# Optimization experiments

Measured on AMD Instinct MI355X. Metric: run time of the kernel, lower is better.

The kernel has to match this reference:

```python
import jax, jax.numpy as jnp
import numpy as np

NEG_INF = -1e9


def _gru_cell(x, h, W_ih, W_hh, b_ih, b_hh):
    # torch GRUCell math, gate order [r; z; n]
    gx = x @ W_ih.T + b_ih          # [B, 3H]
    gh = h @ W_hh.T + b_hh          # [B, 3H]
    xr, xz, xn = jnp.split(gx, 3, axis=-1)
    hr, hz, hn = jnp.split(gh, 3, axis=-1)
    r = jax.nn.sigmoid(xr + hr)
    z = jax.nn.sigmoid(xz + hz)
    n = jnp.tanh(xn + r * hn)
    return (1.0 - z) * n + z * h


def setup_inputs() -> dict:
    key = jax.random.key(0)
    ks = jax.random.split(key, 8)
    B, N, D, H, P = 64, 2048, 256, 256, 256
    s = 0.05
    return {
        "sequence": jax.random.normal(ks[0], (B, N, D), jnp.float32),
        "hidden_t": jax.random.normal(ks[1], (B, H), jnp.float32),
        "sequence_mask": jnp.ones((B, N), jnp.float32),
        "num_steps": 2,
        "W_seq": jax.random.normal(ks[2], (D, P), jnp.float32) * s,
        "W_h": jax.random.normal(ks[3], (H, P), jnp.float32) * s,
        "v_att": jax.random.normal(ks[4], (P,), jnp.float32) * s,
        "W_ih": jax.random.normal(ks[5], (3 * H, D), jnp.float32) * s,
        "W_hh": jax.random.normal(ks[6], (3 * H, H), jnp.float32) * s,
        "b_ih": jnp.zeros((3 * H,), jnp.float32),
        "b_hh": jnp.zeros((3 * H,), jnp.float32),
    }


def reference(sequence, hidden_t, sequence_mask, num_steps,
              W_seq, W_h, v_att, W_ih, W_hh, b_ih, b_hh):
    # Precompute the sequence projection once (invariant across decode steps).
    seq_proj = jnp.einsum("bnd,dp->bnp", sequence, W_seq)   # [B, N, P]
    mask_bias = jnp.where(sequence_mask > 0, 0.0, NEG_INF)  # [B, N]

    def step(h, _):
        # projection similarity: v . tanh(W1 s_i + W2 h)
        proj = jnp.tanh(seq_proj + (h @ W_h)[:, None, :])   # [B, N, P]
        scores = jnp.einsum("bnp,p->bn", proj, v_att) + mask_bias
        w = jax.nn.softmax(scores, axis=-1)                  # [B, N]
        vec = jnp.einsum("bn,bnd->bd", w, sequence)          # [B, D]
        h_new = _gru_cell(vec, h, W_ih, W_hh, b_ih, b_hh)
        return h_new, w

    _, ws = jax.lax.scan(step, hidden_t, None, length=num_steps)  # [T, B, N]
    return jnp.transpose(ws, (1, 0, 2))                            # [B, T, N]
```

## Files before the change

### kernel.cpp

```cpp
#include <hip/hip_runtime.h>
#include <cstdint>

using u16 = unsigned short;
using u32 = unsigned int;
typedef __attribute__((ext_vector_type(8))) short bf16x8;
typedef __attribute__((ext_vector_type(8))) u16 u16x8;
typedef __attribute__((ext_vector_type(16))) float f32x16;
typedef __attribute__((ext_vector_type(2))) u32 u32x2;
typedef __attribute__((ext_vector_type(4))) u32 u32x4;

#define DEV static __device__ __forceinline__

DEV u16 bf16_rne(float x) {
  u32 u = __float_as_uint(x);
  u32 r = (u + 0x7FFFu + ((u >> 16) & 1u)) >> 16;
  return (u16)r;
}
DEV float bf16f(u16 h) { return __uint_as_float(((u32)h) << 16); }

DEV u32 cvt_pk_bf16(float lo, float hi) {
  u32 d;
  asm("v_cvt_pk_bf16_f32 %0, %1, %2" : "=v"(d) : "v"(lo), "v"(hi));
  return d;
}

DEV float fast_tanh(float x) {
  float e = __expf(2.0f * x);
  return fmaf(-2.0f, __builtin_amdgcn_rcpf(e + 1.0f), 1.0f);
}
DEV float sigmoidf_(float x) {
  return __builtin_amdgcn_rcpf(1.0f + __expf(-x));
}

__global__ __launch_bounds__(256) void prep_all(
    const float* __restrict__ Wseq, const float* __restrict__ Wih,
    const float* __restrict__ Whh, u16* __restrict__ WfG,
    float* __restrict__ WT, float* __restrict__ UT,
    const float* __restrict__ h0, const float* __restrict__ Wh,
    float* __restrict__ hw) {
  const int bid = blockIdx.x, t = threadIdx.x;
  if (bid < 32) {
    const int unit = bid * 4 + (t >> 6);
    const int lane = t & 63, l31 = lane & 31, koct = lane >> 5;
    const int pt8 = unit >> 4, kt = unit & 15;
    u16x8 o;
#pragma unroll
    for (int e = 0; e < 8; ++e)
      o[e] = bf16_rne(
          Wseq[(long)(kt * 16 + koct * 8 + e) * 256 + pt8 * 32 + l31]);
    *(u16x8*)(WfG + (long)unit * 512 + lane * 8) = o;
  } else if (bid < 56) {
    const int gid = bid - 32;
    const float* src = (gid >= 12) ? Whh : Wih;
    float* dst = (gid >= 12) ? UT : WT;
    const int g = (gid % 12) * 64 + (t & 63);
    const int dq = t >> 6;
#pragma unroll 4
    for (int d = dq * 64; d < dq * 64 + 64; ++d)
      dst[(long)d * 768 + g] = src[(long)g * 256 + d];
  } else {
    const int idx = bid - 56;
    const int q = idx & 3, b = idx >> 2;
    __shared__ float sh[256];
    __shared__ float sP[4][64];
    sh[t] = h0[b * 256 + t];
    __syncthreads();
    const int j4 = t & 63, dg = t >> 6;
    const int j = q * 64 + j4;
    float g = 0.f;
#pragma unroll 4
    for (int k = dg * 64; k < dg * 64 + 64; ++k)
      g = fmaf(sh[k], Wh[(long)k * 256 + j], g);
    sP[dg][j4] = g;
    __syncthreads();
    if (t < 64)
      hw[b * 256 + q * 64 + t] = (sP[0][t] + sP[1][t]) + (sP[2][t] + sP[3][t]);
  }
}

__global__ __launch_bounds__(256) void hw_q(const float* __restrict__ h,
                                            const float* __restrict__ Wh,
                                            float* __restrict__ hw) {
  const int q = blockIdx.x, b = blockIdx.y, t = threadIdx.x;
  __shared__ float sh[256];
  __shared__ float sP[4][64];
  sh[t] = h[b * 256 + t];
  __syncthreads();
  const int j4 = t & 63, dg = t >> 6;
  const int j = q * 64 + j4;
  float g = 0.f;
#pragma unroll 4
  for (int k = dg * 64; k < dg * 64 + 64; ++k)
    g = fmaf(sh[k], Wh[(long)k * 256 + j], g);
  sP[dg][j4] = g;
  __syncthreads();
  if (t < 64)
    hw[b * 256 + q * 64 + t] = (sP[0][t] + sP[1][t]) + (sP[2][t] + sP[3][t]);
}

struct EpiSmem {
  float sQ[128][5];
  float se[128];
  float shw[256];
  float svv[256];
  float sredE[2];
};

template <bool FROMLDS>
DEV void epilogue(EpiSmem& sm, const f32x16& a00, const f32x16& a01,
                  const f32x16& a10, const f32x16& a11, const u16* bs,
                  const char* sRb, const float* __restrict__ mask,
                  float* __restrict__ wbuf, float* __restrict__ esum,
                  float* __restrict__ part, long nbase, int esumIdx,
                  long partBase, int t, int lane, int w, int l31, int koct,
                  int pg, int ng) {
  float s0a = 0.f, s0b = 0.f, s0c = 0.f, s0d = 0.f;
  float s1a = 0.f, s1b = 0.f, s1c = 0.f, s1d = 0.f;
#pragma unroll
  for (int r = 0; r < 16; r += 4) {
    const int c0 = (r & 3) + 8 * (r >> 2) + 4 * koct;
    const int c1 = ((r + 1) & 3) + 8 * ((r + 1) >> 2) + 4 * koct;
    const int c2 = ((r + 2) & 3) + 8 * ((r + 2) >> 2) + 4 * koct;
    const int c3 = ((r + 3) & 3) + 8 * ((r + 3) >> 2) + 4 * koct;
    const int p0 = pg * 64 + c0, p1 = pg * 64 + c1, p2 = pg * 64 + c2,
              p3 = pg * 64 + c3;
    s0a = fmaf(sm.svv[p0], fast_tanh(a00[r] + sm.shw[p0]), s0a);
    s0b = fmaf(sm.svv[p1], fast_tanh(a00[r + 1] + sm.shw[p1]), s0b);
    s0c = fmaf(sm.svv[p2], fast_tanh(a00[r + 2] + sm.shw[p2]), s0c);
    s0d = fmaf(sm.svv[p3], fast_tanh(a00[r + 3] + sm.shw[p3]), s0d);
    s1a = fmaf(sm.svv[p0], fast_tanh(a01[r] + sm.shw[p0]), s1a);
    s1b = fmaf(sm.svv[p1], fast_tanh(a01[r + 1] + sm.shw[p1]), s1b);
    s1c = fmaf(sm.svv[p2], fast_tanh(a01[r + 2] + sm.shw[p2]), s1c);
    s1d = fmaf(sm.svv[p3], fast_tanh(a01[r + 3] + sm.shw[p3]), s1d);
  }
#pragma unroll
  for (int r = 0; r < 16; r += 4) {
    const int c0 = (r & 3) + 8 * (r >> 2) + 4 * koct;
    const int c1 = ((r + 1) & 3) + 8 * ((r + 1) >> 2) + 4 * koct;
    const int c2 = ((r + 2) & 3) + 8 * ((r + 2) >> 2) + 4 * koct;
    const int c3 = ((r + 3) & 3) + 8 * ((r + 3) >> 2) + 4 * koct;
    const int p0 = pg * 64 + 32 + c0, p1 = pg * 64 + 32 + c1,
              p2 = pg * 64 + 32 + c2, p3 = pg * 64 + 32 + c3;
    s0a = fmaf(sm.svv[p0], fast_tanh(a10[r] + sm.shw[p0]), s0a);
    s0b = fmaf(sm.svv[p1], fast_tanh(a10[r + 1] + sm.shw[p1]), s0b);
    s0c = fmaf(sm.svv[p2], fast_tanh(a10[r + 2] + sm.shw[p2]), s0c);
    s0d = fmaf(sm.svv[p3], fast_tanh(a10[r + 3] + sm.shw[p3]), s0d);
    s1a = fmaf(sm.svv[p0], fast_tanh(a11[r] + sm.shw[p0]), s1a);
    s1b = fmaf(sm.svv[p1], fast_tanh(a11[r + 1] + sm.shw[p1]), s1b);
    s1c = fmaf(sm.svv[p2], fast_tanh(a11[r + 2] + sm.shw[p2]), s1c);
    s1d = fmaf(sm.svv[p3], fast_tanh(a11[r + 3] + sm.shw[p3]), s1d);
  }
  float sc0 = (s0a + s0b) + (s0c + s0d);
  float sc1 = (s1a + s1b) + (s1c + s1d);
  sc0 += __shfl_xor(sc0, 32, 64);
  sc1 += __shfl_xor(sc1, 32, 64);
  if (koct == 0) {
    sm.sQ[ng * 64 + l31][pg] = sc0;
    sm.sQ[ng * 64 + 32 + l31][pg] = sc1;
  }
  __syncthreads();
  if (t < 128) {
    float s = (sm.sQ[t][0] + sm.sQ[t][1]) + (sm.sQ[t][2] + sm.sQ[t][3]);
    const long n = nbase + t;
    float e = (mask[n] > 0.f) ? __expf(s) : 0.f;
    sm.se[t] = e;
    wbuf[n] = e;
    float s4 = e;
#pragma unroll
    for (int off = 1; off < 64; off <<= 1) s4 += __shfl_xor(s4, off, 64);
    if ((t & 63) == 0) sm.sredE[t >> 6] = s4;
  }
  __syncthreads();
  if (t == 0) esum[esumIdx] = sm.sredE[0] + sm.sredE[1];

#pragma unroll
  for (int kk = 0; kk < 2; ++kk) {
    const int kt = w + kk * 8;
    float vd0 = 0, vd1 = 0, vd2 = 0, vd3 = 0, vd4 = 0, vd5 = 0, vd6 = 0,
          vd7 = 0;
#pragma unroll
    for (int t8 = 0; t8 < 4; ++t8) {
      u16x8 q;
      if constexpr (FROMLDS) {
        const int row = t8 * 32 + l31;
        const int colb = (kt * 16 + koct * 8) * 2;
        q = *(const u16x8*)(sRb + row * 512 + (colb ^ ((row & 31) << 4)));
      } else {
        q = *(const u16x8*)(bs + ((long)(t8 * 16 + kt) * 64 + lane) * 8);
      }
      const float wv = sm.se[t8 * 32 + l31];
      vd0 = fmaf(wv, bf16f((u16)q[0]), vd0);
      vd1 = fmaf(wv, bf16f((u16)q[1]), vd1);
      vd2 = fmaf(wv, bf16f((u16)q[2]), vd2);
      vd3 = fmaf(wv, bf16f((u16)q[3]), vd3);
      vd4 = fmaf(wv, bf16f((u16)q[4]), vd4);
      vd5 = fmaf(wv, bf16f((u16)q[5]), vd5);
      vd6 = fmaf(wv, bf16f((u16)q[6]), vd6);
      vd7 = fmaf(wv, bf16f((u16)q[7]), vd7);
    }
#pragma unroll
    for (int off = 1; off < 32; off <<= 1) {
      vd0 += __shfl_xor(vd0, off, 64);
      vd1 += __shfl_xor(vd1, off, 64);
      vd2 += __shfl_xor(vd2, off, 64);
      vd3 += __shfl_xor(vd3, off, 64);
      vd4 += __shfl_xor(vd4, off, 64);
      vd5 += __shfl_xor(vd5, off, 64);
      vd6 += __shfl_xor(vd6, off, 64);
      vd7 += __shfl_xor(vd7, off, 64);
    }
    if (l31 == 0) {
      float4 o0 = {vd0, vd1, vd2, vd3};
      float4 o1 = {vd4, vd5, vd6, vd7};
      float* pp = part + partBase * 256 + kt * 16 + koct * 8;
      *(float4*)pp = o0;
      *(float4*)(pp + 4) = o1;
    }
  }
}

__global__ __launch_bounds__(512, 4) void step0k(
    const float* __restrict__ seq, u16* __restrict__ seqF,
    const u16* __restrict__ WfG, const float* __restrict__ hwbuf,
    const float* __restrict__ vatt, const float* __restrict__ mask,
    float* __restrict__ wbuf, float* __restrict__ esum,
    float* __restrict__ part, int N, int NCH2, int B) {
  __shared__ __align__(16) u16 sR[32768];
  __shared__ EpiSmem sm;

  const int t = threadIdx.x, lane = t & 63, w = t >> 6;
  const int l31 = lane & 31, koct = lane >> 5;
  const int pg = w >> 1, ng = w & 1;
  const int b = blockIdx.y, ch = blockIdx.x;
  char* sRb = (char*)sR;
  const long chbase = (long)(b * NCH2 + ch) << 15;

  const u16* wa0 = WfG + (long)(pg * 32) * 512 + lane * 8;
  const u16* wa1 = wa0 + 8192;

  {
    const float* src = seq + ((long)b * N + ch * 128) * 256;
#pragma unroll
    for (int i = 0; i < 16; ++i) {
      const int idx = i * 2048 + t * 4;
      float4 x = *(const float4*)(src + idx);
      u32x2 o;
      o[0] = cvt_pk_bf16(x.x, x.y);
      o[1] = cvt_pk_bf16(x.z, x.w);
      const int row = idx >> 8, colb = (idx & 255) * 2;
      *(u32x2*)(sRb + row * 512 + (colb ^ ((row & 31) << 4))) = o;
    }
  }
  if (t < 256) {
    sm.shw[t] = hwbuf[b * 256 + t];
    sm.svv[t] = vatt[t];
  }
  __syncthreads();

  f32x16 a00 = (f32x16)0.f, a01 = (f32x16)0.f, a10 = (f32x16)0.f,
         a11 = (f32x16)0.f;
  {
    const int row0 = ng * 64 + l31, row1 = row0 + 32;
    const char* p0 = sRb + row0 * 512;
    const char* p1 = sRb + row1 * 512;
    const int sw0 = (row0 & 31) << 4, sw1 = (row1 & 31) << 4;
    const int cb = koct * 16;
#pragma unroll 4
    for (int kt = 0; kt < 16; ++kt) {
      bf16x8 af0 = *(const bf16x8*)(wa0 + kt * 512);
      bf16x8 af1 = *(const bf16x8*)(wa1 + kt * 512);
      bf16x8 bf0 = *(const bf16x8*)(p0 + ((kt * 32 + cb) ^ sw0));
      bf16x8 bf1 = *(const bf16x8*)(p1 + ((kt * 32 + cb) ^ sw1));
      a00 = __builtin_amdgcn_mfma_f32_32x32x16_bf16(af0, bf0, a00, 0, 0, 0);
      a01 = __builtin_amdgcn_mfma_f32_32x32x16_bf16(af0, bf1, a01, 0, 0, 0);
      a10 = __builtin_amdgcn_mfma_f32_32x32x16_bf16(af1, bf0, a10, 0, 0, 0);
      a11 = __builtin_amdgcn_mfma_f32_32x32x16_bf16(af1, bf1, a11, 0, 0, 0);
    }
  }

  {
    u16* dst = seqF + chbase;
#pragma unroll
    for (int i = 0; i < 8; ++i) {
      const int uidx = i * 512 + t;
      const int ln = uidx & 63, unit = uidx >> 6;
      const int kt = unit & 15, t8 = unit >> 4;
      const int row = t8 * 32 + (ln & 31);
      const int colb = (kt * 16 + (ln >> 5) * 8) * 2;
      u16x8 v = *(const u16x8*)(sRb + row * 512 + (colb ^ ((row & 31) << 4)));
      *(u16x8*)(dst + (long)uidx * 8) = v;
    }
  }
  __syncthreads();
  epilogue<true>(sm, a00, a01, a10, a11, nullptr, sRb, mask, wbuf, esum, part,
                 (long)b * N + ch * 128, b * NCH2 + ch, (long)ch * B + b, t,
                 lane, w, l31, koct, pg, ng);
}

__global__ __launch_bounds__(512, 4) void step1k(
    const u16* __restrict__ seqF, const u16* __restrict__ WfG,
    const float* __restrict__ hwbuf, const float* __restrict__ vatt,
    const float* __restrict__ mask, float* __restrict__ wbuf,
    float* __restrict__ esum, float* __restrict__ part, int N, int NCH2,
    int B) {
  __shared__ EpiSmem sm;
  const int t = threadIdx.x, lane = t & 63, w = t >> 6;
  const int l31 = lane & 31, koct = lane >> 5;
  const int pg = w >> 1, ng = w & 1;
  const int b = blockIdx.y, ch = blockIdx.x;
  const long chbase = (long)(b * NCH2 + ch) << 15;

  if (t < 256) {
    sm.shw[t] = hwbuf[b * 256 + t];
    sm.svv[t] = vatt[t];
  }

  const u16* bs0 = seqF + chbase + ng * 16384 + lane * 8;
  const u16* bs1 = bs0 + 8192;
  const u16* wa0 = WfG + (long)(pg * 32) * 512 + lane * 8;
  const u16* wa1 = wa0 + 8192;

  f32x16 a00 = (f32x16)0.f, a01 = (f32x16)0.f, a10 = (f32x16)0.f,
         a11 = (f32x16)0.f;

  u16x8 A0c, A1c, B0c, B1c, A0n, A1n, B0n, B1n;
  A0c = *(const u16x8*)(wa0);
  A1c = *(const u16x8*)(wa1);
  B0c = *(const u16x8*)(bs0);
  B1c = *(const u16x8*)(bs1);

#define MFMA4(A0, A1, B0, B1)                                                  \
  {                                                                            \
    bf16x8 af0 = *(bf16x8*)&A0, af1 = *(bf16x8*)&A1;                           \
    bf16x8 bf0 = *(bf16x8*)&B0, bf1 = *(bf16x8*)&B1;                           \
    a00 = __builtin_amdgcn_mfma_f32_32x32x16_bf16(af0, bf0, a00, 0, 0, 0);     \
    a01 = __builtin_amdgcn_mfma_f32_32x32x16_bf16(af0, bf1, a01, 0, 0, 0);     \
    a10 = __builtin_amdgcn_mfma_f32_32x32x16_bf16(af1, bf0, a10, 0, 0, 0);     \
    a11 = __builtin_amdgcn_mfma_f32_32x32x16_bf16(af1, bf1, a11, 0, 0, 0);     \
  }

#pragma unroll
  for (int kt2 = 0; kt2 < 8; ++kt2) {
    const int kn = kt2 * 2 + 1;
    A0n = *(const u16x8*)(wa0 + kn * 512);
    A1n = *(const u16x8*)(wa1 + kn * 512);
    B0n = *(const u16x8*)(bs0 + kn * 512);
    B1n = *(const u16x8*)(bs1 + kn * 512);
    MFMA4(A0c, A1c, B0c, B1c);
    if (kt2 < 7) {
      const int kc = kt2 * 2 + 2;
      A0c = *(const u16x8*)(wa0 + kc * 512);
      A1c = *(const u16x8*)(wa1 + kc * 512);
      B0c = *(const u16x8*)(bs0 + kc * 512);
      B1c = *(const u16x8*)(bs1 + kc * 512);
    }
    MFMA4(A0n, A1n, B0n, B1n);
  }
#undef MFMA4

  __syncthreads();
  epilogue<false>(sm, a00, a01, a10, a11, seqF + chbase, nullptr, mask, wbuf,
                  esum, part, (long)b * N + ch * 128, b * NCH2 + ch,
                  (long)ch * B + b, t, lane, w, l31, koct, pg, ng);
}

__global__ __launch_bounds__(256) void finalize_gru(
    const float* __restrict__ part, const float* __restrict__ esumP, int ecnt,
    const float* __restrict__ hprev, const float* __restrict__ WT,
    const float* __restrict__ UT, const float* __restrict__ bih,
    const float* __restrict__ bhh, const float* __restrict__ wbuf,
    float* __restrict__ out, float* __restrict__ hnew, int N, int T, int step,
    int NP, int B) {
  const int q = blockIdx.x, b = blockIdx.y, t = threadIdx.x;
  __shared__ float sv[256], sh[256], sP[6][4][64];
  float S = 0.f;
  for (int i = 0; i < ecnt; ++i) S += esumP[b * ecnt + i];
  const float inv = __builtin_amdgcn_rcpf(S);
  float a = 0.f;
  for (int cc = 0; cc < NP; ++cc) a += part[((long)cc * B + b) * 256 + t];
  sv[t] = a * inv;
  sh[t] = hprev[b * 256 + t];
  __syncthreads();
  const int j4 = t & 63, dg = t >> 6;
  const int j = q * 64 + j4;
  float g0 = 0, g1 = 0, g2 = 0, g3 = 0, g4 = 0, g5 = 0;
#pragma unroll 4
  for (int d = dg * 64; d < dg * 64 + 64; ++d) {
    const float vd = sv[d], hd = sh[d];
    const float* wr_ = WT + (long)d * 768 + j;
    const float* ur_ = UT + (long)d * 768 + j;
    g0 = fmaf(vd, wr_[0], g0);
    g1 = fmaf(vd, wr_[256], g1);
    g2 = fmaf(vd, wr_[512], g2);
    g3 = fmaf(hd, ur_[0], g3);
    g4 = fmaf(hd, ur_[256], g4);
    g5 = fmaf(hd, ur_[512], g5);
  }
  sP[0][dg][j4] = g0;
  sP[1][dg][j4] = g1;
  sP[2][dg][j4] = g2;
  sP[3][dg][j4] = g3;
  sP[4][dg][j4] = g4;
  sP[5][dg][j4] = g5;
  __syncthreads();
  if (t < 64) {
    const int jj = q * 64 + t;
    float xr = bih[jj], xz = bih[256 + jj], xn = bih[512 + jj];
    float hr = bhh[jj], hz = bhh[256 + jj], hn = bhh[512 + jj];
#pragma unroll
    for (int dgg = 0; dgg < 4; ++dgg) {
      xr += sP[0][dgg][t];
      xz += sP[1][dgg][t];
      xn += sP[2][dgg][t];
      hr += sP[3][dgg][t];
      hz += sP[4][dgg][t];
      hn += sP[5][dgg][t];
    }
    float rr = sigmoidf_(xr + hr);
    float zz = sigmoidf_(xz + hz);
    float nn = fast_tanh(xn + rr * hn);
    hnew[b * 256 + jj] = (1.f - zz) * nn + zz * sh[jj];
  }
  const long ob = ((long)b * T + step) * N;
  const int nq = N >> 2;
  for (int i = 0; i * 256 < nq; ++i) {
    const int n = q * nq + i * 256 + t;
    out[ob + n] = wbuf[(long)b * N + n] * inv;
  }
}

extern "C" void kernel_launch(void* const* d_in, const int* in_sizes, int n_in,
                              void* d_out, int out_size, void* d_ws,
                              size_t ws_size, hipStream_t stream) {
  (void)n_in;
  (void)ws_size;
  const float* seq = (const float*)d_in[0];
  const float* hidden = (const float*)d_in[1];
  const float* mask = (const float*)d_in[2];
  const float* Wseq = (const float*)d_in[4];
  const float* Wh = (const float*)d_in[5];
  const float* vatt = (const float*)d_in[6];
  const float* Wih = (const float*)d_in[7];
  const float* Whh = (const float*)d_in[8];
  const float* bih = (const float*)d_in[9];
  const float* bhh = (const float*)d_in[10];
  float* out = (float*)d_out;

  const int P = in_sizes[6];
  const int H = in_sizes[5] / P;
  const int B = in_sizes[1] / H;
  const int N = in_sizes[2] / B;
  const int T = out_size / (B * N);
  const long M = (long)B * N;
  const int NCH2 = N / 128;

  char* p = (char*)d_ws;
  auto alloc = [&](size_t bytes) {
    char* r = p;
    p += (bytes + 255) & ~(size_t)255;
    return r;
  };
  u16* seqF = (u16*)alloc((size_t)M * 256 * 2);
  u16* WfG = (u16*)alloc((size_t)256 * 256 * 2);
  float* WT = (float*)alloc((size_t)256 * 768 * 4);
  float* UT = (float*)alloc((size_t)256 * 768 * 4);
  float* wbuf = (float*)alloc((size_t)B * N * 4);
  float* hwbuf = (float*)alloc((size_t)B * 256 * 4);
  float* hA = (float*)alloc((size_t)B * 256 * 4);
  float* hB = (float*)alloc((size_t)B * 256 * 4);
  float* part = (float*)alloc((size_t)NCH2 * B * 256 * 4);
  float* esum = (float*)alloc((size_t)B * NCH2 * 4);
  float* hbuf[2] = {hA, hB};

  prep_all<<<dim3(56 + 4 * B), dim3(256), 0, stream>>>(
      Wseq, Wih, Whh, WfG, WT, UT, hidden, Wh, hwbuf);

  for (int t = 0; t < T; ++t) {
    const float* hcur = (t == 0) ? hidden : hbuf[(t - 1) & 1];
    if (t > 0) {
      hw_q<<<dim3(4, B), dim3(256), 0, stream>>>(hcur, Wh, hwbuf);
    }
    if (t == 0) {
      step0k<<<dim3(NCH2, B), dim3(512), 0, stream>>>(
          seq, seqF, WfG, hwbuf, vatt, mask, wbuf, esum, part, N, NCH2, B);
    } else {
      step1k<<<dim3(NCH2, B), dim3(512), 0, stream>>>(
          seqF, WfG, hwbuf, vatt, mask, wbuf, esum, part, N, NCH2, B);
    }
    finalize_gru<<<dim3(4, B), dim3(256), 0, stream>>>(
        part, esum, NCH2, hcur, WT, UT, bih, bhh, wbuf, out, hbuf[t & 1], N, T,
        t, NCH2, B);
  }
}
```

Measured before the change: 141.7 us.

## Split step0 K-dimension in halves to overlap second-half loads with first-half MFMA

The step0 kernel now loads and converts only the first half of each sequence row (columns 0-127) into LDS before the MFMA loop. It issues global loads for the second half into registers, runs MFMAs over the first eight k-tiles, writes out the first half of seqF, then converts and stores the second half and runs the remaining k-tiles. The goal is to hide global load latency behind tensor-core work. The eight extra float4 registers per thread lead to the occupancy hint in launch_bounds dropping from 4 to 2, which may reduce the latency hiding the hardware can do across waves.

```diff
diff --git a/kernel.cpp b/kernel.cpp
--- a/kernel.cpp
+++ b/kernel.cpp
@@ -219,7 +219,7 @@
   }
 }
 
-__global__ __launch_bounds__(512, 4) void step0k(
+__global__ __launch_bounds__(512, 2) void step0k(
     const float* __restrict__ seq, u16* __restrict__ seqF,
     const u16* __restrict__ WfG, const float* __restrict__ hwbuf,
     const float* __restrict__ vatt, const float* __restrict__ mask,
@@ -237,19 +237,19 @@
 
   const u16* wa0 = WfG + (long)(pg * 32) * 512 + lane * 8;
   const u16* wa1 = wa0 + 8192;
-
-  {
-    const float* src = seq + ((long)b * N + ch * 128) * 256;
-#pragma unroll
-    for (int i = 0; i < 16; ++i) {
-      const int idx = i * 2048 + t * 4;
-      float4 x = *(const float4*)(src + idx);
-      u32x2 o;
-      o[0] = cvt_pk_bf16(x.x, x.y);
-      o[1] = cvt_pk_bf16(x.z, x.w);
-      const int row = idx >> 8, colb = (idx & 255) * 2;
-      *(u32x2*)(sRb + row * 512 + (colb ^ ((row & 31) << 4))) = o;
-    }
+  const float* src = seq + ((long)b * N + ch * 128) * 256;
+  u16* dst = seqF + chbase;
+
+#pragma unroll
+  for (int i = 0; i < 8; ++i) {
+    const int j = i * 512 + t;
+    const int row = j >> 5, c4 = j & 31;
+    float4 x = *(const float4*)(src + (long)row * 256 + c4 * 4);
+    u32x2 o;
+    o[0] = cvt_pk_bf16(x.x, x.y);
+    o[1] = cvt_pk_bf16(x.z, x.w);
+    const int colb = c4 * 8;
+    *(u32x2*)(sRb + row * 512 + (colb ^ ((row & 31) << 4))) = o;
   }
   if (t < 256) {
     sm.shw[t] = hwbuf[b * 256 + t];
@@ -257,39 +257,87 @@
   }
   __syncthreads();
 
+  float4 y0 = *(const float4*)(src + (long)((0 * 512 + t) >> 5) * 256 +
+                               (((0 * 512 + t) & 31) + 32) * 4);
+  float4 y1 = *(const float4*)(src + (long)((1 * 512 + t) >> 5) * 256 +
+                               (((1 * 512 + t) & 31) + 32) * 4);
+  float4 y2 = *(const float4*)(src + (long)((2 * 512 + t) >> 5) * 256 +
+                               (((2 * 512 + t) & 31) + 32) * 4);
+  float4 y3 = *(const float4*)(src + (long)((3 * 512 + t) >> 5) * 256 +
+                               (((3 * 512 + t) & 31) + 32) * 4);
+  float4 y4 = *(const float4*)(src + (long)((4 * 512 + t) >> 5) * 256 +
+                               (((4 * 512 + t) & 31) + 32) * 4);
+  float4 y5 = *(const float4*)(src + (long)((5 * 512 + t) >> 5) * 256 +
+                               (((5 * 512 + t) & 31) + 32) * 4);
+  float4 y6 = *(const float4*)(src + (long)((6 * 512 + t) >> 5) * 256 +
+                               (((6 * 512 + t) & 31) + 32) * 4);
+  float4 y7 = *(const float4*)(src + (long)((7 * 512 + t) >> 5) * 256 +
+                               (((7 * 512 + t) & 31) + 32) * 4);
+
   f32x16 a00 = (f32x16)0.f, a01 = (f32x16)0.f, a10 = (f32x16)0.f,
          a11 = (f32x16)0.f;
-  {
-    const int row0 = ng * 64 + l31, row1 = row0 + 32;
-    const char* p0 = sRb + row0 * 512;
-    const char* p1 = sRb + row1 * 512;
-    const int sw0 = (row0 & 31) << 4, sw1 = (row1 & 31) << 4;
-    const int cb = koct * 16;
+  const int row0 = ng * 64 + l31, row1 = row0 + 32;
+  const char* p0 = sRb + row0 * 512;
+  const char* p1 = sRb + row1 * 512;
+  const int sw0 = (row0 & 31) << 4, sw1 = (row1 & 31) << 4;
+  const int cb = koct * 16;
 #pragma unroll 4
-    for (int kt = 0; kt < 16; ++kt) {
-      bf16x8 af0 = *(const bf16x8*)(wa0 + kt * 512);
-      bf16x8 af1 = *(const bf16x8*)(wa1 + kt * 512);
-      bf16x8 bf0 = *(const bf16x8*)(p0 + ((kt * 32 + cb) ^ sw0));
-      bf16x8 bf1 = *(const bf16x8*)(p1 + ((kt * 32 + cb) ^ sw1));
-      a00 = __builtin_amdgcn_mfma_f32_32x32x16_bf16(af0, bf0, a00, 0, 0, 0);
-      a01 = __builtin_amdgcn_mfma_f32_32x32x16_bf16(af0, bf1, a01, 0, 0, 0);
-      a10 = __builtin_amdgcn_mfma_f32_32x32x16_bf16(af1, bf0, a10, 0, 0, 0);
-      a11 = __builtin_amdgcn_mfma_f32_32x32x16_bf16(af1, bf1, a11, 0, 0, 0);
-    }
-  }
-
-  {
-    u16* dst = seqF + chbase;
-#pragma unroll
-    for (int i = 0; i < 8; ++i) {
-      const int uidx = i * 512 + t;
-      const int ln = uidx & 63, unit = uidx >> 6;
-      const int kt = unit & 15, t8 = unit >> 4;
-      const int row = t8 * 32 + (ln & 31);
-      const int colb = (kt * 16 + (ln >> 5) * 8) * 2;
-      u16x8 v = *(const u16x8*)(sRb + row * 512 + (colb ^ ((row & 31) << 4)));
-      *(u16x8*)(dst + (long)uidx * 8) = v;
-    }
+  for (int kt = 0; kt < 8; ++kt) {
+    bf16x8 af0 = *(const bf16x8*)(wa0 + kt * 512);
+    bf16x8 af1 = *(const bf16x8*)(wa1 + kt * 512);
+    bf16x8 bf0 = *(const bf16x8*)(p0 + ((kt * 32 + cb) ^ sw0));
+    bf16x8 bf1 = *(const bf16x8*)(p1 + ((kt * 32 + cb) ^ sw1));
+    a00 = __builtin_amdgcn_mfma_f32_32x32x16_bf16(af0, bf0, a00, 0, 0, 0);
+    a01 = __builtin_amdgcn_mfma_f32_32x32x16_bf16(af0, bf1, a01, 0, 0, 0);
+    a10 = __builtin_amdgcn_mfma_f32_32x32x16_bf16(af1, bf0, a10, 0, 0, 0);
+    a11 = __builtin_amdgcn_mfma_f32_32x32x16_bf16(af1, bf1, a11, 0, 0, 0);
+  }
+#pragma unroll
+  for (int i = 0; i < 4; ++i) {
+    const int j = i * 512 + t;
+    const int ln = j & 63, u = j >> 6;
+    const int t8 = u >> 3, kt = u & 7;
+    const int row = t8 * 32 + (ln & 31);
+    const int colb = (kt * 16 + (ln >> 5) * 8) * 2;
+    u16x8 v = *(const u16x8*)(sRb + row * 512 + (colb ^ ((row & 31) << 4)));
+    *(u16x8*)(dst + (long)(t8 * 16 + kt) * 512 + ln * 8) = v;
+  }
+
+#define STOREY(YY, ii)                                                        \
+  {                                                                           \
+    const int j = (ii) * 512 + t;                                             \
+    const int row = j >> 5, c4 = (j & 31) + 32;                               \
+    u32x2 o;                                                                  \
+    o[0] = cvt_pk_bf16(YY.x, YY.y);                                           \
+    o[1] = cvt_pk_bf16(YY.z, YY.w);                                           \
+    const int colb = c4 * 8;                                                  \
+    *(u32x2*)(sRb + row * 512 + (colb ^ ((row & 31) << 4))) = o;              \
+  }
+  STOREY(y0, 0) STOREY(y1, 1) STOREY(y2, 2) STOREY(y3, 3)
+  STOREY(y4, 4) STOREY(y5, 5) STOREY(y6, 6) STOREY(y7, 7)
+#undef STOREY
+  __syncthreads();
+
+#pragma unroll 4
+  for (int kt = 8; kt < 16; ++kt) {
+    bf16x8 af0 = *(const bf16x8*)(wa0 + kt * 512);
+    bf16x8 af1 = *(const bf16x8*)(wa1 + kt * 512);
+    bf16x8 bf0 = *(const bf16x8*)(p0 + ((kt * 32 + cb) ^ sw0));
+    bf16x8 bf1 = *(const bf16x8*)(p1 + ((kt * 32 + cb) ^ sw1));
+    a00 = __builtin_amdgcn_mfma_f32_32x32x16_bf16(af0, bf0, a00, 0, 0, 0);
+    a01 = __builtin_amdgcn_mfma_f32_32x32x16_bf16(af0, bf1, a01, 0, 0, 0);
+    a10 = __builtin_amdgcn_mfma_f32_32x32x16_bf16(af1, bf0, a10, 0, 0, 0);
+    a11 = __builtin_amdgcn_mfma_f32_32x32x16_bf16(af1, bf1, a11, 0, 0, 0);
+  }
+#pragma unroll
+  for (int i = 0; i < 4; ++i) {
+    const int j = i * 512 + t;
+    const int ln = j & 63, u = j >> 6;
+    const int t8 = u >> 3, kt = (u & 7) + 8;
+    const int row = t8 * 32 + (ln & 31);
+    const int colb = (kt * 16 + (ln >> 5) * 8) * 2;
+    u16x8 v = *(const u16x8*)(sRb + row * 512 + (colb ^ ((row & 31) << 4)));
+    *(u16x8*)(dst + (long)(t8 * 16 + kt) * 512 + ln * 8) = v;
   }
   __syncthreads();
   epilogue<true>(sm, a00, a01, a10, a11, nullptr, sRb, mask, wbuf, esum, part,
```

Result: slower. 156.4 us (+10.3%).
